# Performance work log

Measured on AMD Instinct MI355X. Metric: run time of the kernel, lower is better.

## Reference

```python
import jax, jax.numpy as jnp
import numpy as np


def force_fn(x):
    # Harmonic force F = -grad U, U(x) = 0.5 * ||x||^2 (Ornstein-Uhlenbeck).
    return -x


def setup_inputs() -> dict:
    key = jax.random.key(0)
    x0 = jax.random.normal(key, (100000, 3), dtype=jnp.float32)
    return {
        "x0": x0,
        "gamma": jnp.ones((1,), dtype=jnp.float32),
        "kT": jnp.ones((1,), dtype=jnp.float32),
        "dt": jnp.ones((1,), dtype=jnp.float32) * 0.01,
        "n_steps": 1000,
        "store_every": 10,
    }


def reference(x0, gamma, kT, dt, n_steps, store_every):
    # Overdamped Langevin: x_{t+1} = x_t + F(x_t)/gamma * dt + sqrt(2*kT*dt/gamma) * N(0, I)
    gamma_s = gamma.reshape(())
    kT_s = kT.reshape(())
    dt_s = dt.reshape(())
    noise_scale = jnp.sqrt(2.0 * kT_s * dt_s / gamma_s)

    n_chunks = n_steps // store_every  # trajectory stored every `store_every` steps
    keys = jax.random.split(jax.random.key(42), n_chunks * store_every)
    keys = keys.reshape((n_chunks, store_every))

    def step(x, k):
        noise = jax.random.normal(k, x.shape, x.dtype)
        x_new = x + force_fn(x) / gamma_s * dt_s + noise_scale * noise
        return x_new, None

    def chunk(x, ks):
        x, _ = jax.lax.scan(step, x, ks)
        return x, x  # carry and store the state after each chunk

    _, traj = jax.lax.scan(chunk, x0, keys)  # (n_chunks, N, 3)
    return jnp.concatenate([x0[None], traj], axis=0)  # (n_chunks + 1, N, 3)
```

## Files before the change

### kernel.cpp

```cpp
#include <hip/hip_runtime.h>


#define KCAP 1024

__device__ __forceinline__ void tf2x32(unsigned k0, unsigned k1,
                                       unsigned x0, unsigned x1,
                                       unsigned &o0, unsigned &o1) {
    const unsigned ks2 = k0 ^ k1 ^ 0x1BD11BDAu;
    x0 += k0; x1 += k1;
#define RND(r) { x0 += x1; x1 = __builtin_rotateleft32(x1, r); x1 ^= x0; }
    RND(13) RND(15) RND(26) RND(6)
    x0 += k1;  x1 += ks2 + 1u;
    RND(17) RND(29) RND(16) RND(24)
    x0 += ks2; x1 += k0 + 2u;
    RND(13) RND(15) RND(26) RND(6)
    x0 += k0;  x1 += k1 + 3u;
    RND(17) RND(29) RND(16) RND(24)
    x0 += k1;  x1 += ks2 + 4u;
    RND(13) RND(15) RND(26) RND(6)
    x0 += ks2; x1 += k0 + 5u;
#undef RND
    o0 = x0; o1 = x1;
}

__device__ __forceinline__ float bits_to_normal(unsigned bits) {
    const float LO = -0.99999994f;
#if __has_builtin(__builtin_amdgcn_alignbit)
    unsigned fb = __builtin_amdgcn_alignbit(0x7Fu, bits, 9u);
#else
    unsigned fb = (bits >> 9) | 0x3f800000u;
#endif
    float f = __uint_as_float(fb) - 1.0f;
    float u = fmaf(f, 2.0f, LO);
    u = fmaxf(u, LO);
    float w = -__logf(fmaf(-u, u, 1.0f));
    float p;
    if (w < 5.0f) {
        w = w - 2.5f;
        p =              2.81022636e-08f;
        p = fmaf(p, w,   3.43273939e-07f);
        p = fmaf(p, w,  -3.5233877e-06f);
        p = fmaf(p, w,  -4.39150654e-06f);
        p = fmaf(p, w,   0.00021858087f);
        p = fmaf(p, w,  -0.00125372503f);
        p = fmaf(p, w,  -0.00417768164f);
        p = fmaf(p, w,   0.246640727f);
        p = fmaf(p, w,   1.50140941f);
    } else {
        w = sqrtf(w) - 3.0f;
        p =             -0.000200214257f;
        p = fmaf(p, w,   0.000100950558f);
        p = fmaf(p, w,   0.00134934322f);
        p = fmaf(p, w,  -0.00367342844f);
        p = fmaf(p, w,   0.00573950773f);
        p = fmaf(p, w,  -0.0076224613f);
        p = fmaf(p, w,   0.00943887047f);
        p = fmaf(p, w,   1.00167406f);
        p = fmaf(p, w,   2.83297682f);
    }
    return 1.41421356f * (p * u);
}

__device__ __forceinline__ float lang_step(float x, unsigned k0, unsigned k1,
                                           unsigned ks2, unsigned t,
                                           float scale, float na) {
    unsigned x0 = k0, x1 = k1 + t;
#define RND(r) { x0 += x1; x1 = __builtin_rotateleft32(x1, r); x1 ^= x0; }
    RND(13) RND(15) RND(26) RND(6)
    x0 += k1;  x1 += ks2 + 1u;
    RND(17) RND(29) RND(16) RND(24)
    x0 += ks2; x1 += k0 + 2u;
    RND(13) RND(15) RND(26) RND(6)
    x0 += k0;  x1 += k1 + 3u;
    RND(17) RND(29) RND(16) RND(24)
    x0 += k1;  x1 += ks2 + 4u;
    RND(13) RND(15) RND(26) RND(6)
    x0 += ks2; x1 += k0 + 5u;
#undef RND
    float n = bits_to_normal(x0 ^ x1);
    return fmaf(scale, n, fmaf(na, x, x));
}

__global__ __launch_bounds__(256) void OverdampedLangevin_62362925138458_kernel(
    const float* __restrict__ x0,
    const float* __restrict__ gamma_p,
    const float* __restrict__ kT_p,
    const float* __restrict__ dt_p,
    const int*   __restrict__ nsteps_p,
    const int*   __restrict__ store_p,
    float*       __restrict__ out,
    int E)
{
    __shared__ uint4 ksh[KCAP];
    const int n_steps = *nsteps_p;
    const int store_every = *store_p;

    const int nk = n_steps < KCAP ? n_steps : KCAP;
    for (int j = threadIdx.x; j < nk; j += blockDim.x) {
        unsigned b0, b1;
        tf2x32(0u, 42u, 0u, (unsigned)j, b0, b1);
        ksh[j] = make_uint4(b0, b1, b0 ^ b1 ^ 0x1BD11BDAu, 0u);
    }
    __syncthreads();

    const unsigned t = blockIdx.x * blockDim.x + threadIdx.x;
    if ((int)t >= E) return;

    const float g  = gamma_p[0];
    const float kT = kT_p[0];
    const float dt = dt_p[0];
    const float scale = sqrtf(2.0f * kT * dt / g);
    const float na = -(dt / g);

    float x = x0[t];
    out[t] = x;

    if (store_every == 10 && n_steps % 10 == 0 && n_steps <= KCAP) {
        const int n_chunks = n_steps / 10;
        float* op = out + (size_t)E + t;
        const uint4* kp = ksh;
        for (int c = 0; c < n_chunks; ++c) {
#pragma unroll
            for (int s = 0; s < 10; ++s) {
                const uint4 k = kp[s];
                x = lang_step(x, k.x, k.y, k.z, t, scale, na);
            }
            kp += 10;
            *op = x;
            op += (size_t)E;
        }
    } else {
        int frame = 1, since = 0;
#pragma unroll 1
        for (int s = 0; s < n_steps; ++s) {
            unsigned k0, k1, ks2;
            if (s < KCAP) { uint4 k = ksh[s]; k0 = k.x; k1 = k.y; ks2 = k.z; }
            else {
                tf2x32(0u, 42u, 0u, (unsigned)s, k0, k1);
                ks2 = k0 ^ k1 ^ 0x1BD11BDAu;
            }
            x = lang_step(x, k0, k1, ks2, t, scale, na);
            if (++since == store_every) {
                since = 0;
                out[(size_t)frame * (size_t)E + t] = x;
                ++frame;
            }
        }
    }
}

extern "C" void kernel_launch(void* const* d_in, const int* in_sizes, int n_in,
                              void* d_out, int out_size, void* d_ws, size_t ws_size,
                              hipStream_t stream) {
    const float* x0    = (const float*)d_in[0];
    const float* gam   = (const float*)d_in[1];
    const float* kT    = (const float*)d_in[2];
    const float* dt    = (const float*)d_in[3];
    const int*   nst   = (const int*)d_in[4];
    const int*   sev   = (const int*)d_in[5];
    float*       out   = (float*)d_out;

    const int E = in_sizes[0];
    const int blocks = (E + 255) / 256;
    OverdampedLangevin_62362925138458_kernel<<<blocks, 256, 0, stream>>>(
        x0, gam, kT, dt, nst, sev, out, E);
}
```

Measured before the change: 779.6 us.

## Precompute step keys in workspace, fold first Threefry round, use wave-uniform erfinv branch

Moves the per-step Threefry key expansion out of every block into a small pre-kernel that writes the keys to workspace, and reads them from global memory with uniform indices, avoiding the per-block LDS fill and barrier. Precomputes k0+k1 so the first Threefry round collapses, folds the sqrt(2) into the noise scale, and computes the log with a native log2 intrinsic. The erfinv tail branch now takes the cheap path unless any lane in the wave needs it. In exchange it adds a second kernel launch and depends on the workspace being large enough, otherwise it falls back to the shared-memory path.

Result: faster. 723.3 us (-7.2%).

```diff
diff --git a/kernel.cpp b/kernel.cpp
--- a/kernel.cpp
+++ b/kernel.cpp
@@ -2,13 +2,17 @@
 
 
 #define KCAP 1024
+
+__device__ __forceinline__ unsigned rotl(unsigned v, int r) {
+    return __builtin_rotateleft32(v, r);
+}
 
 __device__ __forceinline__ void tf2x32(unsigned k0, unsigned k1,
                                        unsigned x0, unsigned x1,
                                        unsigned &o0, unsigned &o1) {
     const unsigned ks2 = k0 ^ k1 ^ 0x1BD11BDAu;
     x0 += k0; x1 += k1;
-#define RND(r) { x0 += x1; x1 = __builtin_rotateleft32(x1, r); x1 ^= x0; }
+#define RND(r) { x0 += x1; x1 = rotl(x1, r); x1 ^= x0; }
     RND(13) RND(15) RND(26) RND(6)
     x0 += k1;  x1 += ks2 + 1u;
     RND(17) RND(29) RND(16) RND(24)
@@ -23,85 +27,106 @@
     o0 = x0; o1 = x1;
 }
 
-__device__ __forceinline__ float bits_to_normal(unsigned bits) {
-    const float LO = -0.99999994f;
-#if __has_builtin(__builtin_amdgcn_alignbit)
-    unsigned fb = __builtin_amdgcn_alignbit(0x7Fu, bits, 9u);
+__device__ __forceinline__ float poly_lo(float w) {
+    float p =        2.81022636e-08f;
+    p = fmaf(p, w,   3.43273939e-07f);
+    p = fmaf(p, w,  -3.5233877e-06f);
+    p = fmaf(p, w,  -4.39150654e-06f);
+    p = fmaf(p, w,   0.00021858087f);
+    p = fmaf(p, w,  -0.00125372503f);
+    p = fmaf(p, w,  -0.00417768164f);
+    p = fmaf(p, w,   0.246640727f);
+    p = fmaf(p, w,   1.50140941f);
+    return p;
+}
+__device__ __forceinline__ float poly_hi(float s) {
+    float p =       -0.000200214257f;
+    p = fmaf(p, s,   0.000100950558f);
+    p = fmaf(p, s,   0.00134934322f);
+    p = fmaf(p, s,  -0.00367342844f);
+    p = fmaf(p, s,   0.00573950773f);
+    p = fmaf(p, s,  -0.0076224613f);
+    p = fmaf(p, s,   0.00943887047f);
+    p = fmaf(p, s,   1.00167406f);
+    p = fmaf(p, s,   2.83297682f);
+    return p;
+}
+
+__device__ __forceinline__ float lang_step(float x, uint4 k, unsigned t,
+                                           float scale2, float na) {
+    unsigned x1 = k.y + t;
+    unsigned x0 = k.w + t;
+    x1 = rotl(x1, 13) ^ x0;
+#define RND(r) { x0 += x1; x1 = rotl(x1, r); x1 ^= x0; }
+    RND(15) RND(26) RND(6)
+    x0 += k.y; x1 += k.z + 1u;
+    RND(17) RND(29) RND(16) RND(24)
+    x0 += k.z; x1 += k.x + 2u;
+    RND(13) RND(15) RND(26) RND(6)
+    x0 += k.x; x1 += k.y + 3u;
+    RND(17) RND(29) RND(16) RND(24)
+    x0 += k.y; x1 += k.z + 4u;
+    RND(13) RND(15) RND(26) RND(6)
+    x0 += k.z; x1 += k.x + 5u;
+#undef RND
+    unsigned bits = x0 ^ x1;
+
+    unsigned fb = (bits >> 9) | 0x3f800000u;
+    float F = __uint_as_float(fb);
+    float u = fmaf(F, 2.0f, -3.0f);
+    u = fmaxf(u, -0.99999994f);
+    float h = fmaf(-u, u, 1.0f);
+#if __has_builtin(__builtin_amdgcn_logf)
+    float l2 = __builtin_amdgcn_logf(h);
 #else
-    unsigned fb = (bits >> 9) | 0x3f800000u;
+    float l2 = __log2f(h);
 #endif
-    float f = __uint_as_float(fb) - 1.0f;
-    float u = fmaf(f, 2.0f, LO);
-    u = fmaxf(u, LO);
-    float w = -__logf(fmaf(-u, u, 1.0f));
     float p;
-    if (w < 5.0f) {
-        w = w - 2.5f;
-        p =              2.81022636e-08f;
-        p = fmaf(p, w,   3.43273939e-07f);
-        p = fmaf(p, w,  -3.5233877e-06f);
-        p = fmaf(p, w,  -4.39150654e-06f);
-        p = fmaf(p, w,   0.00021858087f);
-        p = fmaf(p, w,  -0.00125372503f);
-        p = fmaf(p, w,  -0.00417768164f);
-        p = fmaf(p, w,   0.246640727f);
-        p = fmaf(p, w,   1.50140941f);
+    if (__builtin_expect(__any(l2 <= -7.2134752f), 0)) {
+        float w  = l2 * -0.69314718f;
+        float p1 = poly_lo(w - 2.5f);
+        float p2 = poly_hi(sqrtf(w) - 3.0f);
+        p = (l2 > -7.2134752f) ? p1 : p2;
     } else {
-        w = sqrtf(w) - 3.0f;
-        p =             -0.000200214257f;
-        p = fmaf(p, w,   0.000100950558f);
-        p = fmaf(p, w,   0.00134934322f);
-        p = fmaf(p, w,  -0.00367342844f);
-        p = fmaf(p, w,   0.00573950773f);
-        p = fmaf(p, w,  -0.0076224613f);
-        p = fmaf(p, w,   0.00943887047f);
-        p = fmaf(p, w,   1.00167406f);
-        p = fmaf(p, w,   2.83297682f);
-    }
-    return 1.41421356f * (p * u);
-}
-
-__device__ __forceinline__ float lang_step(float x, unsigned k0, unsigned k1,
-                                           unsigned ks2, unsigned t,
-                                           float scale, float na) {
-    unsigned x0 = k0, x1 = k1 + t;
-#define RND(r) { x0 += x1; x1 = __builtin_rotateleft32(x1, r); x1 ^= x0; }
-    RND(13) RND(15) RND(26) RND(6)
-    x0 += k1;  x1 += ks2 + 1u;
-    RND(17) RND(29) RND(16) RND(24)
-    x0 += ks2; x1 += k0 + 2u;
-    RND(13) RND(15) RND(26) RND(6)
-    x0 += k0;  x1 += k1 + 3u;
-    RND(17) RND(29) RND(16) RND(24)
-    x0 += k1;  x1 += ks2 + 4u;
-    RND(13) RND(15) RND(26) RND(6)
-    x0 += ks2; x1 += k0 + 5u;
-#undef RND
-    float n = bits_to_normal(x0 ^ x1);
-    return fmaf(scale, n, fmaf(na, x, x));
-}
-
+        p = poly_lo(fmaf(l2, -0.69314718f, -2.5f));
+    }
+    return fmaf(scale2, p * u, fmaf(na, x, x));
+}
+
+__global__ __launch_bounds__(256) void expand_keys(uint4* __restrict__ kw) {
+    unsigned j = blockIdx.x * 256 + threadIdx.x;
+    if (j < KCAP) {
+        unsigned b0, b1;
+        tf2x32(0u, 42u, 0u, j, b0, b1);
+        kw[j] = make_uint4(b0, b1, b0 ^ b1 ^ 0x1BD11BDAu, b0 + b1);
+    }
+}
+
+template <bool GK>
 __global__ __launch_bounds__(256) void OverdampedLangevin_62362925138458_kernel(
-    const float* __restrict__ x0,
+    const float* __restrict__ x0p,
     const float* __restrict__ gamma_p,
     const float* __restrict__ kT_p,
     const float* __restrict__ dt_p,
     const int*   __restrict__ nsteps_p,
     const int*   __restrict__ store_p,
+    const uint4* __restrict__ kw,
     float*       __restrict__ out,
     int E)
 {
-    __shared__ uint4 ksh[KCAP];
+    extern __shared__ uint4 ksh[];
     const int n_steps = *nsteps_p;
     const int store_every = *store_p;
 
-    const int nk = n_steps < KCAP ? n_steps : KCAP;
-    for (int j = threadIdx.x; j < nk; j += blockDim.x) {
-        unsigned b0, b1;
-        tf2x32(0u, 42u, 0u, (unsigned)j, b0, b1);
-        ksh[j] = make_uint4(b0, b1, b0 ^ b1 ^ 0x1BD11BDAu, 0u);
-    }
-    __syncthreads();
+    if (!GK) {
+        const int nk = n_steps < KCAP ? n_steps : KCAP;
+        for (int j = threadIdx.x; j < nk; j += blockDim.x) {
+            unsigned b0, b1;
+            tf2x32(0u, 42u, 0u, (unsigned)j, b0, b1);
+            ksh[j] = make_uint4(b0, b1, b0 ^ b1 ^ 0x1BD11BDAu, b0 + b1);
+        }
+        __syncthreads();
+    }
 
     const unsigned t = blockIdx.x * blockDim.x + threadIdx.x;
     if ((int)t >= E) return;
@@ -109,23 +134,23 @@
     const float g  = gamma_p[0];
     const float kT = kT_p[0];
     const float dt = dt_p[0];
-    const float scale = sqrtf(2.0f * kT * dt / g);
+    const float scale2 = sqrtf(2.0f * kT * dt / g) * 1.41421356f;
     const float na = -(dt / g);
 
-    float x = x0[t];
+    float x = x0p[t];
     out[t] = x;
 
     if (store_every == 10 && n_steps % 10 == 0 && n_steps <= KCAP) {
-        const int n_chunks = n_steps / 10;
+        const int nc = n_steps / 10;
         float* op = out + (size_t)E + t;
-        const uint4* kp = ksh;
-        for (int c = 0; c < n_chunks; ++c) {
+        int idx = 0;
+        for (int c = 0; c < nc; ++c) {
 #pragma unroll
             for (int s = 0; s < 10; ++s) {
-                const uint4 k = kp[s];
-                x = lang_step(x, k.x, k.y, k.z, t, scale, na);
+                const uint4 k = GK ? kw[idx + s] : ksh[idx + s];
+                x = lang_step(x, k, t, scale2, na);
             }
-            kp += 10;
+            idx += 10;
             *op = x;
             op += (size_t)E;
         }
@@ -133,13 +158,14 @@
         int frame = 1, since = 0;
 #pragma unroll 1
         for (int s = 0; s < n_steps; ++s) {
-            unsigned k0, k1, ks2;
-            if (s < KCAP) { uint4 k = ksh[s]; k0 = k.x; k1 = k.y; ks2 = k.z; }
+            uint4 k;
+            if (s < KCAP) k = GK ? kw[s] : ksh[s];
             else {
-                tf2x32(0u, 42u, 0u, (unsigned)s, k0, k1);
-                ks2 = k0 ^ k1 ^ 0x1BD11BDAu;
+                unsigned b0, b1;
+                tf2x32(0u, 42u, 0u, (unsigned)s, b0, b1);
+                k = make_uint4(b0, b1, b0 ^ b1 ^ 0x1BD11BDAu, b0 + b1);
             }
-            x = lang_step(x, k0, k1, ks2, t, scale, na);
+            x = lang_step(x, k, t, scale2, na);
             if (++since == store_every) {
                 since = 0;
                 out[(size_t)frame * (size_t)E + t] = x;
@@ -162,6 +188,15 @@
 
     const int E = in_sizes[0];
     const int blocks = (E + 255) / 256;
-    OverdampedLangevin_62362925138458_kernel<<<blocks, 256, 0, stream>>>(
-        x0, gam, kT, dt, nst, sev, out, E);
-}
+
+    if (ws_size >= KCAP * sizeof(uint4)) {
+        uint4* kw = (uint4*)d_ws;
+        expand_keys<<<(KCAP + 255) / 256, 256, 0, stream>>>(kw);
+        OverdampedLangevin_62362925138458_kernel<true><<<blocks, 256, 0, stream>>>(
+            x0, gam, kT, dt, nst, sev, kw, out, E);
+    } else {
+        OverdampedLangevin_62362925138458_kernel<false>
+            <<<blocks, 256, KCAP * sizeof(uint4), stream>>>(
+            x0, gam, kT, dt, nst, sev, nullptr, out, E);
+    }
+}
```
